# Performance work log

Measured on AMD Instinct MI355X. Metric: run time of the kernel, lower is better.

Reference implementation:

```python
import jax, jax.numpy as jnp
import numpy as np

N = 100000   # nodes
E = 3200000  # edges
C = 256      # in_channels
H = 64       # hidden_channels
G = 512      # graphs in batch
FC = [128, 64, 32, 16]
OUT = 2
EPS = 1e-5


def _linear(key, fan_in, fan_out):
    k1, k2 = jax.random.split(key)
    s = 1.0 / np.sqrt(fan_in)
    W = jax.random.uniform(k1, (fan_in, fan_out), jnp.float32, -s, s)
    b = jax.random.uniform(k2, (fan_out,), jnp.float32, -s, s)
    return W, b


def setup_inputs() -> dict:
    key = jax.random.key(0)
    ks = jax.random.split(key, 12)
    x = jax.random.normal(ks[0], (N, C), jnp.float32)
    edge_index = jax.random.randint(ks[1], (2, E), 0, N, dtype=jnp.int64)
    batch = jnp.sort(jax.random.randint(ks[2], (N,), 0, G, dtype=jnp.int64))
    w1, b1 = _linear(ks[3], C, H)
    w2, b2 = _linear(ks[4], H, H)
    g1 = jnp.ones((H,), jnp.float32); be1 = jnp.zeros((H,), jnp.float32)
    g2 = jnp.ones((H,), jnp.float32); be2 = jnp.zeros((H,), jnp.float32)
    fw1, fb1 = _linear(ks[5], H, FC[0])
    fw2, fb2 = _linear(ks[6], FC[0], FC[1])
    fw3, fb3 = _linear(ks[7], FC[1], FC[2])
    fw4, fb4 = _linear(ks[8], FC[2], FC[3])
    ow, ob = _linear(ks[9], FC[3], OUT)
    return dict(x=x, edge_index=edge_index, batch=batch,
                w1=w1, b1=b1, w2=w2, b2=b2,
                g1=g1, be1=be1, g2=g2, be2=be2,
                fw1=fw1, fb1=fb1, fw2=fw2, fb2=fb2,
                fw3=fw3, fb3=fb3, fw4=fw4, fb4=fb4,
                ow=ow, ob=ob)


def _gcn_layers(x, edge_index, w1, b1, w2, b2, g1, be1, g2, be2):
    # PyG GCNConv: add self loops, symmetric deg^-1/2 normalization, scatter-add at dst
    loops = jnp.arange(N, dtype=edge_index.dtype)
    src = jnp.concatenate([edge_index[0], loops])
    dst = jnp.concatenate([edge_index[1], loops])
    deg = jax.ops.segment_sum(jnp.ones((E + N,), jnp.float32), dst, num_segments=N)
    dis = jnp.where(deg > 0, jax.lax.rsqrt(jnp.maximum(deg, 1.0)), 0.0)
    norm = (dis[src] * dis[dst])[:, None]  # [E+N, 1]

    def conv(h, W, b):
        h = h @ W
        return jax.ops.segment_sum(h[src] * norm, dst, num_segments=N) + b

    def bn(h, g, be):  # BatchNorm1d over node dim (training-mode batch stats)
        m = jnp.mean(h, axis=0)
        v = jnp.var(h, axis=0)
        return (h - m) * jax.lax.rsqrt(v + EPS) * g + be

    h = bn(jax.nn.relu(conv(x, w1, b1)), g1, be1)   # dropout = identity (eval)
    h = bn(jax.nn.relu(conv(h, w2, b2)), g2, be2)
    return h


def reference(x, edge_index, batch, w1, b1, w2, b2, g1, be1, g2, be2,
              fw1, fb1, fw2, fb2, fw3, fb3, fw4, fb4, ow, ob):
    h = _gcn_layers(x, edge_index, w1, b1, w2, b2, g1, be1, g2, be2)
    # global_mean_pool over batch vector
    s = jax.ops.segment_sum(h, batch, num_segments=G)
    cnt = jax.ops.segment_sum(jnp.ones((N,), jnp.float32), batch, num_segments=G)
    p = s / jnp.maximum(cnt, 1.0)[:, None]  # [G, H]
    h = jax.nn.relu(p @ fw1 + fb1)
    h = jax.nn.relu(h @ fw2 + fb2)
    h = jax.nn.relu(h @ fw3 + fb3)
    h = jax.nn.relu(h @ fw4 + fb4)
    return h @ ow + ob  # [G, OUT]
```

## Files before the change

### kernel.cpp

```cpp
#include <hip/hip_runtime.h>
#include <hip/hip_fp16.h>

#define N_NODES 100000
#define E_EDGES 3200000
#define NG      512
#define BN_EPS  1e-5f

#define BSH     7
#define BNODES  128
#define NBUCK   782
#define NCHUNK  1024
#define CHUNK   3125

__global__ __launch_bounds__(256) void k_zero(float* __restrict__ stats1,
                                              float* __restrict__ stats2,
                                              float* __restrict__ sums,
                                              float* __restrict__ cnt) {
  int i = blockIdx.x * 256 + threadIdx.x;
  if (i < 128) { stats1[i] = 0.f; stats2[i] = 0.f; }
  if (i < NG * 64) sums[i] = 0.f;
  if (i < NG) cnt[i] = 0.f;
}

__global__ __launch_bounds__(256) void kb_hist(const int* __restrict__ ei,
                                               int* __restrict__ counts) {
  __shared__ int h[NBUCK];
  const int c = blockIdx.x, tid = threadIdx.x;
  for (int b = tid; b < NBUCK; b += 256) h[b] = 0;
  __syncthreads();
  const int* dst = ei + E_EDGES + c * CHUNK;
  for (int i = tid; i < CHUNK; i += 256) atomicAdd(&h[dst[i] >> BSH], 1);
  __syncthreads();
  for (int b = tid; b < NBUCK; b += 256) counts[b * NCHUNK + c] = h[b];
}

__global__ __launch_bounds__(1024) void kb_scan1(int* __restrict__ counts,
                                                 int* __restrict__ btot) {
  __shared__ int sm[NCHUNK];
  const int b = blockIdx.x, tid = threadIdx.x;
  const int cval = counts[b * NCHUNK + tid];
  int val = cval;
  sm[tid] = val;
  __syncthreads();
  for (int off = 1; off < NCHUNK; off <<= 1) {
    int t = (tid >= off) ? sm[tid - off] : 0;
    __syncthreads();
    val += t;
    sm[tid] = val;
    __syncthreads();
  }
  counts[b * NCHUNK + tid] = val - cval;
  if (tid == NCHUNK - 1) btot[b] = val;
}

__global__ __launch_bounds__(1024) void kb_scan2(const int* __restrict__ btot,
                                                 int* __restrict__ bbase) {
  __shared__ int sm[1024];
  const int tid = threadIdx.x;
  const int cval = (tid < NBUCK) ? btot[tid] : 0;
  int val = cval;
  sm[tid] = val;
  __syncthreads();
  for (int off = 1; off < 1024; off <<= 1) {
    int t = (tid >= off) ? sm[tid - off] : 0;
    __syncthreads();
    val += t;
    sm[tid] = val;
    __syncthreads();
  }
  if (tid < NBUCK) bbase[tid] = val - cval;
  if (tid == NBUCK - 1) bbase[NBUCK] = val;
}

__global__ __launch_bounds__(256) void kb_scatter(const int* __restrict__ ei,
                                                  const int* __restrict__ counts,
                                                  const int* __restrict__ bbase,
                                                  int* __restrict__ binned) {
  __shared__ int cur[NBUCK];
  const int c = blockIdx.x, tid = threadIdx.x;
  for (int b = tid; b < NBUCK; b += 256) cur[b] = bbase[b] + counts[b * NCHUNK + c];
  __syncthreads();
  const int* srcp = ei + c * CHUNK;
  const int* dstp = ei + E_EDGES + c * CHUNK;
  for (int i = tid; i < CHUNK; i += 256) {
    const int s = srcp[i], d = dstp[i];
    const int pos = atomicAdd(&cur[d >> BSH], 1);
    binned[pos] = ((d & (BNODES - 1)) << 17) | s;
  }
}

__global__ __launch_bounds__(256) void kb_degsort(const int* __restrict__ binned,
                                                  const int* __restrict__ bbase,
                                                  int* __restrict__ csr,
                                                  int* __restrict__ row_start,
                                                  float* __restrict__ dis) {
  __shared__ int h[BNODES];
  __shared__ int pre[BNODES];
  const int b = blockIdx.x, tid = threadIdx.x;
  if (tid < BNODES) h[tid] = 0;
  __syncthreads();
  const int e0 = bbase[b], e1 = bbase[b + 1];
  for (int i = e0 + tid; i < e1; i += 256) atomicAdd(&h[binned[i] >> 17], 1);
  __syncthreads();
  if (tid < BNODES) pre[tid] = h[tid];
  __syncthreads();
  for (int off = 1; off < BNODES; off <<= 1) {
    int t = (tid >= off && tid < BNODES) ? pre[tid - off] : 0;
    __syncthreads();
    if (tid < BNODES) pre[tid] += t;
    __syncthreads();
  }
  if (tid < BNODES) {
    const int n = b * BNODES + tid;
    const int ex = e0 + pre[tid] - h[tid];
    if (n < N_NODES) {
      row_start[n] = ex;
      dis[n] = rsqrtf((float)(h[tid] + 1));
    }
    h[tid] = ex;
  }
  if (b == NBUCK - 1 && tid == 0) row_start[N_NODES] = E_EDGES;
  __syncthreads();
  for (int i = e0 + tid; i < e1; i += 256) {
    const int v = binned[i];
    const int pos = atomicAdd(&h[v >> 17], 1);
    csr[pos] = v & 0x1FFFF;
  }
}

template <int K, bool BN>
__global__ __launch_bounds__(256) void k_gemm(const float* __restrict__ in,
                                              const float* __restrict__ W,
                                              const float* __restrict__ dis,
                                              const float* __restrict__ stats,
                                              const float* __restrict__ gam,
                                              const float* __restrict__ bet,
                                              __half* __restrict__ y) {
  __shared__ float xs[64 * 68];
  __shared__ float wsm[64 * 64];
  __shared__ float scv[64], shv[64];
  const int tid = threadIdx.x;
  const int n0 = blockIdx.x * 64;
  const int lane = tid & 63, wv = tid >> 6;
  const int nq = lane & 15;
  const int chb = wv * 16 + (lane >> 4) * 4;
  if (BN) {
    if (tid < 64) {
      const float m = stats[tid] * (1.0f / N_NODES);
      const float v = stats[64 + tid] * (1.0f / N_NODES) - m * m;
      const float sc = rsqrtf(v + BN_EPS) * gam[tid];
      scv[tid] = sc;
      shv[tid] = bet[tid] - m * sc;
    }
  }
  float a[4][4] = {{0,0,0,0},{0,0,0,0},{0,0,0,0},{0,0,0,0}};
  for (int c0 = 0; c0 < K; c0 += 64) {
    __syncthreads();
#pragma unroll
    for (int i = 0; i < 4; ++i) {
      const int idx = tid + i * 256;
      const int n = idx >> 4, c4 = (idx & 15) * 4;
      const int nn = min(n0 + n, N_NODES - 1);
      float4 v = *(const float4*)&in[(size_t)nn * K + c0 + c4];
      if (BN) {
        v.x = v.x * scv[c4] + shv[c4];
        v.y = v.y * scv[c4 + 1] + shv[c4 + 1];
        v.z = v.z * scv[c4 + 2] + shv[c4 + 2];
        v.w = v.w * scv[c4 + 3] + shv[c4 + 3];
      }
      *(float4*)&xs[n * 68 + c4] = v;
    }
#pragma unroll
    for (int i = 0; i < 4; ++i) {
      const int idx = tid + i * 256;
      const int c = idx >> 4, ch4 = (idx & 15) * 4;
      *(float4*)&wsm[c * 64 + ch4] = *(const float4*)&W[(size_t)(c0 + c) * 64 + ch4];
    }
    __syncthreads();
    for (int c = 0; c < 64; c += 4) {
      float wq[4][4];
#pragma unroll
      for (int cc = 0; cc < 4; ++cc) {
        const float4 w4 = *(const float4*)&wsm[(c + cc) * 64 + chb];
        wq[cc][0] = w4.x; wq[cc][1] = w4.y; wq[cc][2] = w4.z; wq[cc][3] = w4.w;
      }
#pragma unroll
      for (int i = 0; i < 4; ++i) {
        const float4 xv = *(const float4*)&xs[(nq + 16 * i) * 68 + c];
#pragma unroll
        for (int j = 0; j < 4; ++j) {
          a[i][j] = fmaf(xv.x, wq[0][j],
                    fmaf(xv.y, wq[1][j],
                    fmaf(xv.z, wq[2][j],
                    fmaf(xv.w, wq[3][j], a[i][j]))));
        }
      }
    }
  }
#pragma unroll
  for (int i = 0; i < 4; ++i) {
    const int n = n0 + nq + 16 * i;
    if (n < N_NODES) {
      const float d = dis[n];
      union { __half h[4]; float2 f; } u;
      u.h[0] = __float2half_rn(d * a[i][0]);
      u.h[1] = __float2half_rn(d * a[i][1]);
      u.h[2] = __float2half_rn(d * a[i][2]);
      u.h[3] = __float2half_rn(d * a[i][3]);
      *(float2*)&y[((size_t)wv * N_NODES + n) * 16 + (lane >> 4) * 4] = u.f;
    }
  }
}

template <bool POOL>
__global__ __launch_bounds__(256) void k_gather(const int* __restrict__ csr,
                                                const int* __restrict__ rs,
                                                const __half* __restrict__ y,
                                                const float* __restrict__ dis,
                                                const float* __restrict__ bias,
                                                float* __restrict__ hout,
                                                float* __restrict__ stats,
                                                const int* __restrict__ batch,
                                                float* __restrict__ sums,
                                                float* __restrict__ cnt) {
  const int tid  = threadIdx.x;
  const int lane = tid & 63;
  const int slot = lane >> 2;
  const int cq   = lane & 3;
  const int slice = (blockIdx.x & 7) >> 1;
  const int sbase = slice * 16;
  const int chl  = cq * 4 + (slot & 3);
  const int ch   = sbase + chl;
  const int j    = ((blockIdx.x >> 3) << 1) | (blockIdx.x & 1);
  const int wid  = j * 4 + (tid >> 6);
  const int per  = (N_NODES + 2047) / 2048;
  const int n0   = wid * per;
  const int n1   = min(N_NODES, n0 + per);
  const float bch = bias[ch];
  const __half* yb = y + (size_t)slice * N_NODES * 16 + cq * 4;
  float s1 = 0.f, s2 = 0.f;
  int curg = -1, run = 0;
  float px = 0.f;
  union U4 { float2 f2; __half2 h2[2]; };
  for (int n = n0; n < n1; ++n) {
    int e = rs[n];
    const int end = rs[n + 1];
    float a0 = 0.f, a1 = 0.f, a2 = 0.f, a3 = 0.f;
    if (slot == 0) {
      U4 u;
      u.f2 = *(const float2*)&yb[(size_t)n * 16];
      const float2 f0 = __half22float2(u.h2[0]);
      const float2 f1 = __half22float2(u.h2[1]);
      a0 += f0.x; a1 += f0.y; a2 += f1.x; a3 += f1.y;
    }
    for (; e + 32 <= end; e += 32) {
      const int ia = __builtin_nontemporal_load(&csr[e + slot]);
      const int ib = __builtin_nontemporal_load(&csr[e + 16 + slot]);
      U4 ua, ub;
      ua.f2 = *(const float2*)&yb[(size_t)ia * 16];
      ub.f2 = *(const float2*)&yb[(size_t)ib * 16];
      const float2 fa0 = __half22float2(ua.h2[0]);
      const float2 fa1 = __half22float2(ua.h2[1]);
      const float2 fb0 = __half22float2(ub.h2[0]);
      const float2 fb1 = __half22float2(ub.h2[1]);
      a0 += fa0.x + fb0.x; a1 += fa0.y + fb0.y;
      a2 += fa1.x + fb1.x; a3 += fa1.y + fb1.y;
    }
    for (; e + 16 <= end; e += 16) {
      const int ia = __builtin_nontemporal_load(&csr[e + slot]);
      U4 ua;
      ua.f2 = *(const float2*)&yb[(size_t)ia * 16];
      const float2 fa0 = __half22float2(ua.h2[0]);
      const float2 fa1 = __half22float2(ua.h2[1]);
      a0 += fa0.x; a1 += fa0.y; a2 += fa1.x; a3 += fa1.y;
    }
    if (e < end) {
      const int rem = end - e;
      const int ia = __builtin_nontemporal_load(&csr[slot < rem ? e + slot : e]);
      U4 u;
      u.f2 = *(const float2*)&yb[(size_t)ia * 16];
      if (slot < rem) {
        const float2 f0 = __half22float2(u.h2[0]);
        const float2 f1 = __half22float2(u.h2[1]);
        a0 += f0.x; a1 += f0.y; a2 += f1.x; a3 += f1.y;
      }
    }
    a0 += __shfl_xor(a0, 32); a1 += __shfl_xor(a1, 32);
    a2 += __shfl_xor(a2, 32); a3 += __shfl_xor(a3, 32);
    a0 += __shfl_xor(a0, 16); a1 += __shfl_xor(a1, 16);
    a2 += __shfl_xor(a2, 16); a3 += __shfl_xor(a3, 16);
    float t0, t1;
    {
      const bool hi = (slot & 2) != 0;
      const float sd0 = hi ? a0 : a2;
      const float sd1 = hi ? a1 : a3;
      const float kp0 = hi ? a2 : a0;
      const float kp1 = hi ? a3 : a1;
      t0 = kp0 + __shfl_xor(sd0, 8);
      t1 = kp1 + __shfl_xor(sd1, 8);
    }
    float s;
    {
      const bool hi = (slot & 1) != 0;
      const float sd = hi ? t0 : t1;
      const float kp = hi ? t1 : t0;
      s = kp + __shfl_xor(sd, 4);
    }
    const float v = fmaxf(dis[n] * s + bch, 0.f);
    if (lane < 16) {
      if (!POOL) __builtin_nontemporal_store(v, &hout[(size_t)n * 64 + ch]);
      s1 += v;
      s2 += v * v;
    }
    if (POOL) {
      const int g = batch[n];
      if (g != curg) {
        if (run) {
          if (lane < 16) atomicAdd(&sums[curg * 64 + ch], px);
          if (lane == 0 && slice == 0) atomicAdd(&cnt[curg], (float)run);
        }
        curg = g; run = 0; px = 0.f;
      }
      if (lane < 16) px += v;
      ++run;
    }
  }
  if (POOL && run) {
    if (lane < 16) atomicAdd(&sums[curg * 64 + ch], px);
    if (lane == 0 && slice == 0) atomicAdd(&cnt[curg], (float)run);
  }
  __shared__ float r1[64], r2[64];
  const int wv = tid >> 6;
  if (lane < 16) {
    r1[wv * 16 + chl] = s1;
    r2[wv * 16 + chl] = s2;
  }
  __syncthreads();
  if (tid < 16) {
    atomicAdd(&stats[sbase + tid], r1[tid] + r1[tid + 16] + r1[tid + 32] + r1[tid + 48]);
  } else if (tid < 32) {
    const int h = tid - 16;
    atomicAdd(&stats[64 + sbase + h], r2[h] + r2[h + 16] + r2[h + 32] + r2[h + 48]);
  }
}

__global__ __launch_bounds__(128) void k_mlp(const float* __restrict__ sums,
                                             const float* __restrict__ cnt,
                                             const float* __restrict__ stats,
                                             const float* __restrict__ gam,
                                             const float* __restrict__ bet,
                                             const float* __restrict__ fw1, const float* __restrict__ fb1,
                                             const float* __restrict__ fw2, const float* __restrict__ fb2,
                                             const float* __restrict__ fw3, const float* __restrict__ fb3,
                                             const float* __restrict__ fw4, const float* __restrict__ fb4,
                                             const float* __restrict__ ow, const float* __restrict__ ob,
                                             float* __restrict__ out) {
  __shared__ float u0[128], u1[128];
  const int g = blockIdx.x, t = threadIdx.x;
  if (t < 64) {
    const float m = stats[t] * (1.0f / N_NODES);
    const float v = stats[64 + t] * (1.0f / N_NODES) - m * m;
    const float sc = rsqrtf(v + BN_EPS) * gam[t];
    const float sh = bet[t] - m * sc;
    u0[t] = (sums[g * 64 + t] / fmaxf(cnt[g], 1.0f)) * sc + sh;
  }
  __syncthreads();
  if (t < 128) {
    float a = fb1[t];
    for (int k = 0; k < 64; ++k) a = fmaf(u0[k], fw1[k * 128 + t], a);
    u1[t] = fmaxf(a, 0.f);
  }
  __syncthreads();
  if (t < 64) {
    float a = fb2[t];
    for (int k = 0; k < 128; ++k) a = fmaf(u1[k], fw2[k * 64 + t], a);
    u0[t] = fmaxf(a, 0.f);
  }
  __syncthreads();
  if (t < 32) {
    float a = fb3[t];
    for (int k = 0; k < 64; ++k) a = fmaf(u0[k], fw3[k * 32 + t], a);
    u1[t] = fmaxf(a, 0.f);
  }
  __syncthreads();
  if (t < 16) {
    float a = fb4[t];
    for (int k = 0; k < 32; ++k) a = fmaf(u1[k], fw4[k * 16 + t], a);
    u0[t] = fmaxf(a, 0.f);
  }
  __syncthreads();
  if (t < 2) {
    float a = ob[t];
    for (int k = 0; k < 16; ++k) a = fmaf(u0[k], ow[k * 2 + t], a);
    out[g * 2 + t] = a;
  }
}

extern "C" void kernel_launch(void* const* d_in, const int* in_sizes, int n_in,
                              void* d_out, int out_size, void* d_ws, size_t ws_size,
                              hipStream_t stream) {
  const float* x    = (const float*)d_in[0];
  const int*   ei   = (const int*)d_in[1];
  const int*   batch= (const int*)d_in[2];
  const float* w1   = (const float*)d_in[3];
  const float* b1   = (const float*)d_in[4];
  const float* w2   = (const float*)d_in[5];
  const float* b2   = (const float*)d_in[6];
  const float* g1   = (const float*)d_in[7];
  const float* be1  = (const float*)d_in[8];
  const float* g2   = (const float*)d_in[9];
  const float* be2  = (const float*)d_in[10];
  const float* fw1  = (const float*)d_in[11]; const float* fb1 = (const float*)d_in[12];
  const float* fw2  = (const float*)d_in[13]; const float* fb2 = (const float*)d_in[14];
  const float* fw3  = (const float*)d_in[15]; const float* fb3 = (const float*)d_in[16];
  const float* fw4  = (const float*)d_in[17]; const float* fb4 = (const float*)d_in[18];
  const float* ow   = (const float*)d_in[19]; const float* ob  = (const float*)d_in[20];
  float* out = (float*)d_out;

  char* ws = (char*)d_ws;
  auto alloc = [&](size_t bytes) {
    void* p = ws;
    ws += (bytes + 255) & ~(size_t)255;
    return p;
  };
  float*  dis      = (float*)alloc((size_t)N_NODES * 4);
  int*    counts   = (int*)  alloc((size_t)NBUCK * NCHUNK * 4);
  int*    btot     = (int*)  alloc((size_t)NBUCK * 4);
  int*    bbase    = (int*)  alloc((size_t)(NBUCK + 1) * 4);
  int*    binned   = (int*)  alloc((size_t)E_EDGES * 4);
  int*    csr      = (int*)  alloc((size_t)E_EDGES * 4);
  int*    row_start= (int*)  alloc((size_t)(N_NODES + 1) * 4);
  __half* yH       = (__half*)alloc((size_t)N_NODES * 64 * 2);
  float*  hB       = (float*)alloc((size_t)N_NODES * 64 * 4);
  float*  stats1   = (float*)alloc(512);
  float*  stats2   = (float*)alloc(512);
  float*  sums     = (float*)alloc((size_t)NG * 64 * 4);
  float*  cnt      = (float*)alloc((size_t)NG * 4);

  const int nblkG = (N_NODES + 63) / 64;

  k_zero    <<<128, 256, 0, stream>>>(stats1, stats2, sums, cnt);
  kb_hist   <<<NCHUNK, 256, 0, stream>>>(ei, counts);
  kb_scan1  <<<NBUCK, NCHUNK, 0, stream>>>(counts, btot);
  kb_scan2  <<<1, 1024, 0, stream>>>(btot, bbase);
  kb_scatter<<<NCHUNK, 256, 0, stream>>>(ei, counts, bbase, binned);
  kb_degsort<<<NBUCK, 256, 0, stream>>>(binned, bbase, csr, row_start, dis);

  k_gemm<256, false><<<nblkG, 256, 0, stream>>>(x, w1, dis, nullptr, nullptr, nullptr, yH);
  k_gather<false><<<2048, 256, 0, stream>>>(csr, row_start, yH, dis, b1, hB, stats1,
                                            nullptr, nullptr, nullptr);

  k_gemm<64, true><<<nblkG, 256, 0, stream>>>(hB, w2, dis, stats1, g1, be1, yH);
  k_gather<true><<<2048, 256, 0, stream>>>(csr, row_start, yH, dis, b2, nullptr, stats2,
                                           batch, sums, cnt);

  k_mlp<<<NG, 128, 0, stream>>>(sums, cnt, stats2, g2, be2,
                                fw1, fb1, fw2, fb2, fw3, fb3, fw4, fb4, ow, ob, out);
}
```

Baseline: 677.4 us.

## Use atomic work queues with XCC-aware slice affinity and software-prefetched CSR indices in gather

Replaces the static per-wave node ranges in the gather kernels with per-slice atomic work queues that hand out 48-node chunks. Each wave starts on the channel slice matching its XCC (read via s_getreg) so that slice's half-precision features tend to stay in that XCC's L2. The edge loop is restructured to prefetch the next 32 CSR indices while the current ones are gathered. BN stats are reduced through shared-memory atomics. The aim is better load balance across skewed degrees and better cache locality, at the cost of queue atomics and some extra control flow.

```diff
diff --git a/kernel.cpp b/kernel.cpp
--- a/kernel.cpp
+++ b/kernel.cpp
@@ -11,15 +11,18 @@
 #define NBUCK   782
 #define NCHUNK  1024
 #define CHUNK   3125
+#define GCH     48
 
 __global__ __launch_bounds__(256) void k_zero(float* __restrict__ stats1,
                                               float* __restrict__ stats2,
                                               float* __restrict__ sums,
-                                              float* __restrict__ cnt) {
+                                              float* __restrict__ cnt,
+                                              int* __restrict__ q) {
   int i = blockIdx.x * 256 + threadIdx.x;
   if (i < 128) { stats1[i] = 0.f; stats2[i] = 0.f; }
   if (i < NG * 64) sums[i] = 0.f;
   if (i < NG) cnt[i] = 0.f;
+  if (i < 8) q[i] = 0;
 }
 
 __global__ __launch_bounds__(256) void kb_hist(const int* __restrict__ ei,
@@ -222,125 +225,136 @@
                                                 float* __restrict__ stats,
                                                 const int* __restrict__ batch,
                                                 float* __restrict__ sums,
-                                                float* __restrict__ cnt) {
+                                                float* __restrict__ cnt,
+                                                int* __restrict__ q,
+                                                const int qbase) {
+  __shared__ float r1sh[64], r2sh[64];
   const int tid  = threadIdx.x;
   const int lane = tid & 63;
   const int slot = lane >> 2;
   const int cq   = lane & 3;
-  const int slice = (blockIdx.x & 7) >> 1;
-  const int sbase = slice * 16;
   const int chl  = cq * 4 + (slot & 3);
-  const int ch   = sbase + chl;
-  const int j    = ((blockIdx.x >> 3) << 1) | (blockIdx.x & 1);
-  const int wid  = j * 4 + (tid >> 6);
-  const int per  = (N_NODES + 2047) / 2048;
-  const int n0   = wid * per;
-  const int n1   = min(N_NODES, n0 + per);
-  const float bch = bias[ch];
-  const __half* yb = y + (size_t)slice * N_NODES * 16 + cq * 4;
-  float s1 = 0.f, s2 = 0.f;
-  int curg = -1, run = 0;
-  float px = 0.f;
+  if (tid < 64) { r1sh[tid] = 0.f; r2sh[tid] = 0.f; }
+  __syncthreads();
+  const int xcc = __builtin_amdgcn_s_getreg(6164) & 7;
+  const int xslice = (xcc >> 1) & 3;
   union U4 { float2 f2; __half2 h2[2]; };
-  for (int n = n0; n < n1; ++n) {
-    int e = rs[n];
-    const int end = rs[n + 1];
-    float a0 = 0.f, a1 = 0.f, a2 = 0.f, a3 = 0.f;
-    if (slot == 0) {
-      U4 u;
-      u.f2 = *(const float2*)&yb[(size_t)n * 16];
-      const float2 f0 = __half22float2(u.h2[0]);
-      const float2 f1 = __half22float2(u.h2[1]);
-      a0 += f0.x; a1 += f0.y; a2 += f1.x; a3 += f1.y;
-    }
-    for (; e + 32 <= end; e += 32) {
-      const int ia = __builtin_nontemporal_load(&csr[e + slot]);
-      const int ib = __builtin_nontemporal_load(&csr[e + 16 + slot]);
-      U4 ua, ub;
-      ua.f2 = *(const float2*)&yb[(size_t)ia * 16];
-      ub.f2 = *(const float2*)&yb[(size_t)ib * 16];
-      const float2 fa0 = __half22float2(ua.h2[0]);
-      const float2 fa1 = __half22float2(ua.h2[1]);
-      const float2 fb0 = __half22float2(ub.h2[0]);
-      const float2 fb1 = __half22float2(ub.h2[1]);
-      a0 += fa0.x + fb0.x; a1 += fa0.y + fb0.y;
-      a2 += fa1.x + fb1.x; a3 += fa1.y + fb1.y;
-    }
-    for (; e + 16 <= end; e += 16) {
-      const int ia = __builtin_nontemporal_load(&csr[e + slot]);
-      U4 ua;
-      ua.f2 = *(const float2*)&yb[(size_t)ia * 16];
-      const float2 fa0 = __half22float2(ua.h2[0]);
-      const float2 fa1 = __half22float2(ua.h2[1]);
-      a0 += fa0.x; a1 += fa0.y; a2 += fa1.x; a3 += fa1.y;
-    }
-    if (e < end) {
-      const int rem = end - e;
-      const int ia = __builtin_nontemporal_load(&csr[slot < rem ? e + slot : e]);
-      U4 u;
-      u.f2 = *(const float2*)&yb[(size_t)ia * 16];
-      if (slot < rem) {
-        const float2 f0 = __half22float2(u.h2[0]);
-        const float2 f1 = __half22float2(u.h2[1]);
-        a0 += f0.x; a1 += f0.y; a2 += f1.x; a3 += f1.y;
-      }
-    }
-    a0 += __shfl_xor(a0, 32); a1 += __shfl_xor(a1, 32);
-    a2 += __shfl_xor(a2, 32); a3 += __shfl_xor(a3, 32);
-    a0 += __shfl_xor(a0, 16); a1 += __shfl_xor(a1, 16);
-    a2 += __shfl_xor(a2, 16); a3 += __shfl_xor(a3, 16);
-    float t0, t1;
-    {
-      const bool hi = (slot & 2) != 0;
-      const float sd0 = hi ? a0 : a2;
-      const float sd1 = hi ? a1 : a3;
-      const float kp0 = hi ? a2 : a0;
-      const float kp1 = hi ? a3 : a1;
-      t0 = kp0 + __shfl_xor(sd0, 8);
-      t1 = kp1 + __shfl_xor(sd1, 8);
-    }
-    float s;
-    {
-      const bool hi = (slot & 1) != 0;
-      const float sd = hi ? t0 : t1;
-      const float kp = hi ? t1 : t0;
-      s = kp + __shfl_xor(sd, 4);
-    }
-    const float v = fmaxf(dis[n] * s + bch, 0.f);
-    if (lane < 16) {
-      if (!POOL) __builtin_nontemporal_store(v, &hout[(size_t)n * 64 + ch]);
-      s1 += v;
-      s2 += v * v;
-    }
-    if (POOL) {
-      const int g = batch[n];
-      if (g != curg) {
-        if (run) {
-          if (lane < 16) atomicAdd(&sums[curg * 64 + ch], px);
-          if (lane == 0 && slice == 0) atomicAdd(&cnt[curg], (float)run);
-        }
-        curg = g; run = 0; px = 0.f;
-      }
-      if (lane < 16) px += v;
-      ++run;
-    }
-  }
-  if (POOL && run) {
-    if (lane < 16) atomicAdd(&sums[curg * 64 + ch], px);
-    if (lane == 0 && slice == 0) atomicAdd(&cnt[curg], (float)run);
-  }
-  __shared__ float r1[64], r2[64];
-  const int wv = tid >> 6;
-  if (lane < 16) {
-    r1[wv * 16 + chl] = s1;
-    r2[wv * 16 + chl] = s2;
-  }
-  __syncthreads();
-  if (tid < 16) {
-    atomicAdd(&stats[sbase + tid], r1[tid] + r1[tid + 16] + r1[tid + 32] + r1[tid + 48]);
-  } else if (tid < 32) {
-    const int h = tid - 16;
-    atomicAdd(&stats[64 + sbase + h], r2[h] + r2[h + 16] + r2[h + 32] + r2[h + 48]);
+  for (int ss = 0; ss < 4; ++ss) {
+    const int sl    = (xslice + ss) & 3;
+    const int sbase = sl * 16;
+    const int ch    = sbase + chl;
+    const float bch = bias[ch];
+    const __half* yb = y + (size_t)sl * N_NODES * 16 + cq * 4;
+    while (true) {
+      int c0;
+      if (lane == 0) c0 = atomicAdd(&q[qbase + sl], GCH);
+      c0 = __shfl(c0, 0);
+      if (c0 >= N_NODES) break;
+      const int c1 = min(N_NODES, c0 + GCH);
+      int pb  = rs[c0];
+      int pfa = __builtin_nontemporal_load(&csr[min(pb + slot, E_EDGES - 1)]);
+      int pfb = __builtin_nontemporal_load(&csr[min(pb + 16 + slot, E_EDGES - 1)]);
+      float s1 = 0.f, s2 = 0.f;
+      int curg = -1, run = 0;
+      float px = 0.f;
+      for (int n = c0; n < c1; ++n) {
+        const int end = rs[n + 1];
+        float a0 = 0.f, a1 = 0.f, a2 = 0.f, a3 = 0.f;
+        if (slot == 0) {
+          U4 u;
+          u.f2 = *(const float2*)&yb[(size_t)n * 16];
+          const float2 f0 = __half22float2(u.h2[0]);
+          const float2 f1 = __half22float2(u.h2[1]);
+          a0 += f0.x; a1 += f0.y; a2 += f1.x; a3 += f1.y;
+        }
+        while (pb < end) {
+          const int rem = end - pb;
+          const int ca = pfa, cb = pfb;
+          pb = (rem > 32) ? pb + 32 : end;
+          pfa = __builtin_nontemporal_load(&csr[min(pb + slot, E_EDGES - 1)]);
+          pfb = __builtin_nontemporal_load(&csr[min(pb + 16 + slot, E_EDGES - 1)]);
+          if (rem >= 32) {
+            U4 ua, ub;
+            ua.f2 = *(const float2*)&yb[(size_t)ca * 16];
+            ub.f2 = *(const float2*)&yb[(size_t)cb * 16];
+            const float2 fa0 = __half22float2(ua.h2[0]);
+            const float2 fa1 = __half22float2(ua.h2[1]);
+            const float2 fb0 = __half22float2(ub.h2[0]);
+            const float2 fb1 = __half22float2(ub.h2[1]);
+            a0 += fa0.x + fb0.x; a1 += fa0.y + fb0.y;
+            a2 += fa1.x + fb1.x; a3 += fa1.y + fb1.y;
+          } else {
+            if (slot < rem) {
+              U4 ua;
+              ua.f2 = *(const float2*)&yb[(size_t)ca * 16];
+              const float2 fa0 = __half22float2(ua.h2[0]);
+              const float2 fa1 = __half22float2(ua.h2[1]);
+              a0 += fa0.x; a1 += fa0.y; a2 += fa1.x; a3 += fa1.y;
+            }
+            if (16 + slot < rem) {
+              U4 ub;
+              ub.f2 = *(const float2*)&yb[(size_t)cb * 16];
+              const float2 fb0 = __half22float2(ub.h2[0]);
+              const float2 fb1 = __half22float2(ub.h2[1]);
+              a0 += fb0.x; a1 += fb0.y; a2 += fb1.x; a3 += fb1.y;
+            }
+          }
+        }
+        a0 += __shfl_xor(a0, 32); a1 += __shfl_xor(a1, 32);
+        a2 += __shfl_xor(a2, 32); a3 += __shfl_xor(a3, 32);
+        a0 += __shfl_xor(a0, 16); a1 += __shfl_xor(a1, 16);
+        a2 += __shfl_xor(a2, 16); a3 += __shfl_xor(a3, 16);
+        float t0, t1;
+        {
+          const bool hi = (slot & 2) != 0;
+          const float sd0 = hi ? a0 : a2;
+          const float sd1 = hi ? a1 : a3;
+          const float kp0 = hi ? a2 : a0;
+          const float kp1 = hi ? a3 : a1;
+          t0 = kp0 + __shfl_xor(sd0, 8);
+          t1 = kp1 + __shfl_xor(sd1, 8);
+        }
+        float s;
+        {
+          const bool hi = (slot & 1) != 0;
+          const float sd = hi ? t0 : t1;
+          const float kp = hi ? t1 : t0;
+          s = kp + __shfl_xor(sd, 4);
+        }
+        const float v = fmaxf(dis[n] * s + bch, 0.f);
+        if (lane < 16) {
+          if (!POOL) __builtin_nontemporal_store(v, &hout[(size_t)n * 64 + ch]);
+          s1 += v;
+          s2 += v * v;
+        }
+        if (POOL) {
+          const int g = batch[n];
+          if (g != curg) {
+            if (run) {
+              if (lane < 16) atomicAdd(&sums[curg * 64 + ch], px);
+              if (lane == 0 && sl == 0) atomicAdd(&cnt[curg], (float)run);
+            }
+            curg = g; run = 0; px = 0.f;
+          }
+          if (lane < 16) px += v;
+          ++run;
+        }
+      }
+      if (POOL && run) {
+        if (lane < 16) atomicAdd(&sums[curg * 64 + ch], px);
+        if (lane == 0 && sl == 0) atomicAdd(&cnt[curg], (float)run);
+      }
+      if (lane < 16) {
+        atomicAdd(&r1sh[ch], s1);
+        atomicAdd(&r2sh[ch], s2);
+      }
+    }
+  }
+  __syncthreads();
+  if (tid < 64) {
+    atomicAdd(&stats[tid], r1sh[tid]);
+  } else if (tid < 128) {
+    atomicAdd(&stats[64 + (tid - 64)], r2sh[tid - 64]);
   }
 }
 
@@ -436,10 +450,11 @@
   float*  stats2   = (float*)alloc(512);
   float*  sums     = (float*)alloc((size_t)NG * 64 * 4);
   float*  cnt      = (float*)alloc((size_t)NG * 4);
+  int*    q        = (int*)  alloc(32);
 
   const int nblkG = (N_NODES + 63) / 64;
 
-  k_zero    <<<128, 256, 0, stream>>>(stats1, stats2, sums, cnt);
+  k_zero    <<<128, 256, 0, stream>>>(stats1, stats2, sums, cnt, q);
   kb_hist   <<<NCHUNK, 256, 0, stream>>>(ei, counts);
   kb_scan1  <<<NBUCK, NCHUNK, 0, stream>>>(counts, btot);
   kb_scan2  <<<1, 1024, 0, stream>>>(btot, bbase);
@@ -448,11 +463,11 @@
 
   k_gemm<256, false><<<nblkG, 256, 0, stream>>>(x, w1, dis, nullptr, nullptr, nullptr, yH);
   k_gather<false><<<2048, 256, 0, stream>>>(csr, row_start, yH, dis, b1, hB, stats1,
-                                            nullptr, nullptr, nullptr);
+                                            nullptr, nullptr, nullptr, q, 0);
 
   k_gemm<64, true><<<nblkG, 256, 0, stream>>>(hB, w2, dis, stats1, g1, be1, yH);
   k_gather<true><<<2048, 256, 0, stream>>>(csr, row_start, yH, dis, b2, nullptr, stats2,
-                                           batch, sums, cnt);
+                                           batch, sums, cnt, q, 4);
 
   k_mlp<<<NG, 128, 0, stream>>>(sums, cnt, stats2, g2, be2,
                                 fw1, fb1, fw2, fb2, fw3, fb3, fw4, fb4, ow, ob, out);
```

After: 1.574 ms. 2.32x slower.
